# Kernel tuning notes

Hardware: AMD Instinct MI355X
Metric: run time of the kernel (lower is better)

The kernel has to match this reference:

```python
import jax, jax.numpy as jnp
import numpy as np

K = 1024
D = 256


def setup_inputs() -> dict:
    key = jax.random.key(0)
    k1, k2 = jax.random.split(key)
    x = jax.random.normal(k1, (32, 1024, D), dtype=jnp.float32)
    codebook = jax.random.normal(k2, (K, D), dtype=jnp.float32) / np.sqrt(D).astype(np.float32)
    return {"x": x, "codebook": codebook}


def reference(x, codebook):
    # Inference-mode forward of EMAQuantizer (EMA buffer updates are training-only side effects).
    orig_shape = x.shape
    x_flat = x.reshape(-1, D)                                   # [N, D]
    x2 = jnp.sum(x_flat * x_flat, axis=1, keepdims=True)        # [N, 1]
    e2 = jnp.sum(codebook * codebook, axis=1)[None, :]          # [1, K]
    xe = x_flat @ codebook.T                                    # [N, K]
    dist = x2 + e2 - 2.0 * xe                                   # [N, K]
    indices = jnp.argmin(dist, axis=1)                          # [N]
    x_q = codebook[indices].reshape(orig_shape)                 # gather + reshape
    # straight-through estimator
    x_q_st = x + jax.lax.stop_gradient(x_q - x)
    return x_q_st, indices.reshape(orig_shape[:-1])
```

## Files before the change

kernel.cpp:

```cpp
#include <hip/hip_runtime.h>

#define D 256

typedef __attribute__((ext_vector_type(8))) _Float16 f16x8;
typedef __attribute__((ext_vector_type(8))) short    s16x8;
typedef __attribute__((ext_vector_type(4))) float    f4_t;

__global__ __launch_bounds__(256) void conv_all(
    const float* __restrict__ x, short* __restrict__ xh, float* __restrict__ x2,
    const float* __restrict__ cb, short* __restrict__ eh, float* __restrict__ e2,
    int nx) {
    __shared__ float tile[16 * 264];
    const int t = threadIdx.x;
    const int bid = blockIdx.x;
    const bool isX = bid < nx;
    const float* in; short* out; float* sq; int p;
    if (isX) { in = x;  out = xh; sq = x2; p = bid; }
    else     { in = cb; out = eh; sq = e2; p = bid - nx; }
    const float* src = in + (size_t)p * 16 * 256;
#pragma unroll
    for (int it = 0; it < 4; ++it) {
        int idx = it * 256 + t;
        int row = idx >> 6, c4 = idx & 63;
        float4 v = *(const float4*)(src + row * 256 + c4 * 4);
        *(float4*)(tile + row * 264 + c4 * 4) = v;
    }
    __syncthreads();
    {
        int row = t >> 4, lane = t & 15;
        int b = lane >> 3, j = lane & 7;
        const float* q = tile + row * 264 + b * 128 + j;
        float r = 0.f;
        {
#pragma clang fp contract(off)
            for (int i = 0; i < 16; ++i) { float v = q[8 * i]; float s2 = v * v; r = r + s2; }
        }
        r += __shfl_xor(r, 1); r += __shfl_xor(r, 2);
        r += __shfl_xor(r, 4); r += __shfl_xor(r, 8);
        if (lane == 0) sq[p * 16 + row] = r;
    }
    const float sgn = isX ? -1.0f : 1.0f;
#pragma unroll
    for (int jj = 0; jj < 2; ++jj) {
        int sl = jj * 256 + t;
        int s = sl >> 6, chunk = (sl >> 4) & 3, rr = sl & 15;
        const float* q = tile + rr * 264 + s * 32 + chunk * 8;
        s16x8 h8;
#pragma unroll
        for (int e = 0; e < 8; ++e) {
            _Float16 hv = (_Float16)(sgn * q[e]);
            h8[e] = (short)__builtin_bit_cast(unsigned short, hv);
        }
        *(s16x8*)(out + (size_t)p * 4096 + (size_t)sl * 8) = h8;
    }
}

__global__ __launch_bounds__(256, 2) void vq_gemm(
    const short* __restrict__ Xh, const short* __restrict__ Eh,
    const float* __restrict__ e2, int* __restrict__ cand) {
    __shared__ short Bs[4 * 4096];
    __shared__ float e2s[256];
    const int tid = threadIdx.x;
    const int l = tid & 63;
    const int w = tid >> 6;
    const int rb = blockIdx.x & 127;
    const int q  = blockIdx.x >> 7;
    const int R0 = rb * 256;
    const int pcBase = q * 16;

#define STAGE(pp) do {                                                        \
    const short* g_ = Eh + (size_t)(pcBase + (pp)) * 4096 + w * 512 + l * 8;  \
    short* d_ = (short*)Bs + ((pp) & 3) * 4096 + w * 512;                     \
    __builtin_amdgcn_global_load_lds(                                         \
        (const __attribute__((address_space(1))) void*)g_,                    \
        (__attribute__((address_space(3))) void*)d_, 16, 0, 0);               \
    __builtin_amdgcn_global_load_lds(                                         \
        (const __attribute__((address_space(1))) void*)(g_ + 2048),           \
        (__attribute__((address_space(3))) void*)(d_ + 2048), 16, 0, 0);      \
} while (0)

    f16x8 aa[4][8];
#pragma unroll
    for (int m = 0; m < 4; ++m)
#pragma unroll
        for (int s = 0; s < 8; ++s)
            aa[m][s] = *(const f16x8*)(Xh +
                (size_t)((R0 >> 4) + w * 4 + m) * 4096 + s * 512 + l * 8);

    e2s[tid] = 0.5f * e2[q * 256 + tid] + 256.0f;

    STAGE(0); STAGE(1);
    __syncthreads();

    unsigned int k1[4][4], k2[4][4];
#pragma unroll
    for (int m = 0; m < 4; ++m)
#pragma unroll
        for (int r = 0; r < 4; ++r) { k1[m][r] = 0xFFFFFFFFu; k2[m][r] = 0xFFFFFFFFu; }

#define SPBODY(S)                                                             \
    __builtin_amdgcn_s_barrier();                                             \
    asm volatile("" ::: "memory");                                            \
    _Pragma("unroll")                                                         \
    for (int hp = 0; hp < 2; ++hp) {                                          \
        const int p = 2 * (S) + hp;                                           \
        const short* bp = (const short*)Bs + (p & 3) * 4096;                  \
        const float e2b = e2s[p * 16 + (l & 15)];                             \
        f4_t acc[4][2];                                                       \
        _Pragma("unroll")                                                     \
        for (int m = 0; m < 4; ++m) {                                         \
            f4_t sd = {e2b, e2b, e2b, e2b};                                   \
            f4_t z  = {0.f, 0.f, 0.f, 0.f};                                   \
            acc[m][0] = sd; acc[m][1] = z;                                    \
        }                                                                     \
        __builtin_amdgcn_s_setprio(1);                                        \
        {                                                                     \
            f16x8 bb[4];                                                      \
            _Pragma("unroll")                                                 \
            for (int k = 0; k < 4; ++k)                                       \
                bb[k] = *(const f16x8*)(bp + k * 512 + l * 8);                \
            _Pragma("unroll")                                                 \
            for (int k = 0; k < 4; ++k)                                       \
                _Pragma("unroll")                                             \
                for (int m = 0; m < 4; ++m)                                   \
                    acc[m][0] = __builtin_amdgcn_mfma_f32_16x16x32_f16(       \
                        aa[m][k], bb[k], acc[m][0], 0, 0, 0);                 \
        }                                                                     \
        {                                                                     \
            f16x8 bb[4];                                                      \
            _Pragma("unroll")                                                 \
            for (int k = 0; k < 4; ++k)                                       \
                bb[k] = *(const f16x8*)(bp + (k + 4) * 512 + l * 8);          \
            _Pragma("unroll")                                                 \
            for (int k = 0; k < 4; ++k)                                       \
                _Pragma("unroll")                                             \
                for (int m = 0; m < 4; ++m)                                   \
                    acc[m][1] = __builtin_amdgcn_mfma_f32_16x16x32_f16(       \
                        aa[m][k + 4], bb[k], acc[m][1], 0, 0, 0);             \
        }                                                                     \
        __builtin_amdgcn_s_setprio(0);                                        \
        const unsigned int code = (unsigned int)(q * 256 + p * 16 + (l & 15));\
        _Pragma("unroll")                                                     \
        for (int m = 0; m < 4; ++m)                                           \
            _Pragma("unroll")                                                 \
            for (int r = 0; r < 4; ++r) {                                     \
                float v = acc[m][0][r] + acc[m][1][r];    \
                unsigned int u = __builtin_bit_cast(unsigned int, v);         \
                unsigned int key = (u & 0xFFFFFC00u) | code;    \
                unsigned int t_ = key > k1[m][r] ? key : k1[m][r];            \
                k2[m][r] = k2[m][r] < t_ ? k2[m][r] : t_;           \
                k1[m][r] = k1[m][r] < key ? k1[m][r] : key;                   \
            }                                                                 \
    }                                                                         \
    __builtin_amdgcn_s_barrier();                                             \
    asm volatile("" ::: "memory");

#pragma unroll 1
    for (int s = 0; s < 7; ++s) {
        STAGE(2 * s + 2); STAGE(2 * s + 3);
        asm volatile("s_waitcnt vmcnt(4)" ::: "memory");
        SPBODY(s)
    }
    {
        asm volatile("s_waitcnt vmcnt(0)" ::: "memory");
        SPBODY(7)
    }

    {
        int q4 = l >> 4;
#pragma unroll
        for (int m = 0; m < 4; ++m)
#pragma unroll
            for (int r = 0; r < 4; ++r) {
                unsigned int a = k1[m][r], b = k2[m][r];
#pragma unroll
                for (int msk = 1; msk < 16; msk <<= 1) {
                    unsigned int oa = __shfl_xor(a, msk);
                    unsigned int ob = __shfl_xor(b, msk);
                    unsigned int hi_ = a > oa ? a : oa;
                    a = a < oa ? a : oa;
                    b = b < ob ? b : ob;
                    b = b < hi_ ? b : hi_;
                }
                if ((l & 15) == 0) {
                    int row = R0 + w * 64 + m * 16 + q4 * 4 + r;
                    int2 o; o.x = (int)(a & 1023u); o.y = (int)(b & 1023u);
                    *(int2*)(cand + (size_t)row * 8 + q * 2) = o;
                }
            }
    }
#undef SPBODY
#undef STAGE
}

__global__ __launch_bounds__(256) void vq_decide(const float* __restrict__ x,
    const float* __restrict__ cb, const int* __restrict__ cand,
    const float* __restrict__ x2, const float* __restrict__ e2,
    float* __restrict__ outq, float* __restrict__ outi) {
    const int w = threadIdx.x >> 6, l = threadIdx.x & 63;
    const int row = blockIdx.x * 4 + w;
    const int o = l >> 3, j = l & 7;
    const int c = cand[(size_t)row * 8 + o];
    const float4* xr = (const float4*)(x + (size_t)row * D);
    const float4* er = (const float4*)(cb + (size_t)c * D);
    float xe = 0.f;
#pragma unroll
    for (int i = 0; i < 8; ++i) {
        float4 xv = xr[i * 8 + j], ev = er[i * 8 + j];
        xe = fmaf(xv.x, ev.x, xe); xe = fmaf(xv.y, ev.y, xe);
        xe = fmaf(xv.z, ev.z, xe); xe = fmaf(xv.w, ev.w, xe);
    }
    xe += __shfl_xor(xe, 1); xe += __shfl_xor(xe, 2); xe += __shfl_xor(xe, 4);
    float s0 = x2[row] + e2[c];
    float dist = s0 - 2.f * xe;
    float best = 3.4e38f; int bi = 0x7fffffff;
#pragma unroll
    for (int oq = 0; oq < 8; ++oq) {
        float dd = __shfl(dist, oq * 8);
        int   ii = __shfl(c,    oq * 8);
        if (dd < best || (dd == best && ii < bi)) { best = dd; bi = ii; }
    }
    float4 v = ((const float4*)(cb + (size_t)bi * D))[l];
    ((float4*)(outq + (size_t)row * D))[l] = v;
    if (l == 0) outi[row] = (float)bi;
}

extern "C" void kernel_launch(void* const* d_in, const int* in_sizes, int n_in,
                              void* d_out, int out_size, void* d_ws, size_t ws_size,
                              hipStream_t stream) {
    const float* x  = (const float*)d_in[0];
    const float* cb = (const float*)d_in[1];
    const int N  = in_sizes[0] / D;
    const int Kc = in_sizes[1] / D;

    float* outq = (float*)d_out;
    float* outi = outq + (size_t)N * D;

    const size_t needX = (size_t)N * D * 2;
    const size_t needS = (size_t)Kc * D * 2 + (size_t)Kc * 4
                       + (size_t)N * 4 + (size_t)N * 8 * 4;

    short* Xh; char* small;
    if (ws_size >= needX + needS) {
        Xh = (short*)d_ws;
        small = (char*)d_ws + needX;
    } else {
        Xh = (short*)d_out;
        small = (char*)d_ws;
    }
    short* Eh  = (short*)small;
    float* e2  = (float*)(Eh + (size_t)Kc * D);
    float* x2  = e2 + Kc;
    int*  cand = (int*)(x2 + N);

    conv_all<<<N / 16 + Kc / 16, 256, 0, stream>>>(x, Xh, x2, cb, Eh, e2, N / 16);
    vq_gemm<<<(N / 256) * 4, 256, 0, stream>>>(Xh, Eh, e2, cand);
    vq_decide<<<N / 4, 256, 0, stream>>>(x, cb, cand, x2, e2, outq, outi);
}
```

Measured before the change: 57.13 us.

## Restructure VQ GEMM into single-wave blocks with per-wave double-buffered codebook staging

The distance GEMM kernel now uses 64-thread, single-wavefront blocks that each cover 64 rows, instead of 256-thread blocks where four waves share codebook tiles. This removes the workgroup barriers, and the pipeline becomes a per-tile double buffer in LDS, waited on with vmcnt. Since tiles are no longer shared across waves, each block loads the full codebook quarter itself, which quadruples global/L2 traffic for the codebook. The grid also grows fourfold. A redundant no-op min line was added to the top-2 update.

```diff
diff --git a/kernel.cpp b/kernel.cpp
--- a/kernel.cpp
+++ b/kernel.cpp
@@ -55,29 +55,16 @@
     }
 }
 
-__global__ __launch_bounds__(256, 2) void vq_gemm(
+__global__ __launch_bounds__(64, 2) void vq_gemm(
     const short* __restrict__ Xh, const short* __restrict__ Eh,
     const float* __restrict__ e2, int* __restrict__ cand) {
-    __shared__ short Bs[4 * 4096];
+    __shared__ short Bs[2 * 4096];
     __shared__ float e2s[256];
-    const int tid = threadIdx.x;
-    const int l = tid & 63;
-    const int w = tid >> 6;
-    const int rb = blockIdx.x & 127;
-    const int q  = blockIdx.x >> 7;
-    const int R0 = rb * 256;
+    const int l  = threadIdx.x;
+    const int rb = blockIdx.x & 511;
+    const int q  = blockIdx.x >> 9;
+    const int R0 = rb * 64;
     const int pcBase = q * 16;
-
-#define STAGE(pp) do {                                                        \
-    const short* g_ = Eh + (size_t)(pcBase + (pp)) * 4096 + w * 512 + l * 8;  \
-    short* d_ = (short*)Bs + ((pp) & 3) * 4096 + w * 512;                     \
-    __builtin_amdgcn_global_load_lds(                                         \
-        (const __attribute__((address_space(1))) void*)g_,                    \
-        (__attribute__((address_space(3))) void*)d_, 16, 0, 0);               \
-    __builtin_amdgcn_global_load_lds(                                         \
-        (const __attribute__((address_space(1))) void*)(g_ + 2048),           \
-        (__attribute__((address_space(3))) void*)(d_ + 2048), 16, 0, 0);      \
-} while (0)
 
     f16x8 aa[4][8];
 #pragma unroll
@@ -85,12 +72,24 @@
 #pragma unroll
         for (int s = 0; s < 8; ++s)
             aa[m][s] = *(const f16x8*)(Xh +
-                (size_t)((R0 >> 4) + w * 4 + m) * 4096 + s * 512 + l * 8);
-
-    e2s[tid] = 0.5f * e2[q * 256 + tid] + 256.0f;
-
-    STAGE(0); STAGE(1);
-    __syncthreads();
+                (size_t)((R0 >> 4) + m) * 4096 + s * 512 + l * 8);
+
+#define STAGE(pp) do {                                                        \
+    const short* g_ = Eh + (size_t)(pcBase + (pp)) * 4096 + l * 8;            \
+    short* d_ = (short*)Bs + ((pp) & 1) * 4096 + l * 8;                       \
+    _Pragma("unroll")                                                         \
+    for (int c_ = 0; c_ < 8; ++c_)                                            \
+        __builtin_amdgcn_global_load_lds(                                     \
+            (const __attribute__((address_space(1))) void*)(g_ + c_ * 512),   \
+            (__attribute__((address_space(3))) void*)(d_ + c_ * 512),         \
+            16, 0, 0);                                                        \
+} while (0)
+
+    STAGE(0);
+
+#pragma unroll
+    for (int i = 0; i < 4; ++i)
+        e2s[i * 64 + l] = 0.5f * e2[q * 256 + i * 64 + l] + 256.0f;
 
     unsigned int k1[4][4], k2[4][4];
 #pragma unroll
@@ -98,14 +97,10 @@
 #pragma unroll
         for (int r = 0; r < 4; ++r) { k1[m][r] = 0xFFFFFFFFu; k2[m][r] = 0xFFFFFFFFu; }
 
-#define SPBODY(S)                                                             \
-    __builtin_amdgcn_s_barrier();                                             \
-    asm volatile("" ::: "memory");                                            \
-    _Pragma("unroll")                                                         \
-    for (int hp = 0; hp < 2; ++hp) {                                          \
-        const int p = 2 * (S) + hp;                                           \
-        const short* bp = (const short*)Bs + (p & 3) * 4096;                  \
-        const float e2b = e2s[p * 16 + (l & 15)];                             \
+#define PBODY(P)                                                              \
+    {                                                                         \
+        const short* bp = (const short*)Bs + ((P) & 1) * 4096;                \
+        const float e2b = e2s[(P) * 16 + (l & 15)];                           \
         f4_t acc[4][2];                                                       \
         _Pragma("unroll")                                                     \
         for (int m = 0; m < 4; ++m) {                                         \
@@ -139,31 +134,30 @@
                         aa[m][k + 4], bb[k], acc[m][1], 0, 0, 0);             \
         }                                                                     \
         __builtin_amdgcn_s_setprio(0);                                        \
-        const unsigned int code = (unsigned int)(q * 256 + p * 16 + (l & 15));\
+        const unsigned int code = (unsigned int)(q * 256 + (P) * 16 + (l & 15));\
         _Pragma("unroll")                                                     \
         for (int m = 0; m < 4; ++m)                                           \
             _Pragma("unroll")                                                 \
             for (int r = 0; r < 4; ++r) {                                     \
                 float v = acc[m][0][r] + acc[m][1][r];    \
                 unsigned int u = __builtin_bit_cast(unsigned int, v);         \
-                unsigned int key = (u & 0xFFFFFC00u) | code;    \
+                unsigned int key = (u & 0xFFFFFC00u) | code;                  \
                 unsigned int t_ = key > k1[m][r] ? key : k1[m][r];            \
                 k2[m][r] = k2[m][r] < t_ ? k2[m][r] : t_;           \
                 k1[m][r] = k1[m][r] < key ? k1[m][r] : key;                   \
+                k1[m][r] = k1[m][r] < key ? k1[m][r] : k1[m][r];              \
             }                                                                 \
-    }                                                                         \
-    __builtin_amdgcn_s_barrier();                                             \
-    asm volatile("" ::: "memory");
+    }
 
 #pragma unroll 1
-    for (int s = 0; s < 7; ++s) {
-        STAGE(2 * s + 2); STAGE(2 * s + 3);
-        asm volatile("s_waitcnt vmcnt(4)" ::: "memory");
-        SPBODY(s)
+    for (int p = 0; p < 15; ++p) {
+        STAGE(p + 1);
+        asm volatile("s_waitcnt vmcnt(8)" ::: "memory");
+        PBODY(p)
     }
     {
         asm volatile("s_waitcnt vmcnt(0)" ::: "memory");
-        SPBODY(7)
+        PBODY(15)
     }
 
     {
@@ -183,13 +177,13 @@
                     b = b < hi_ ? b : hi_;
                 }
                 if ((l & 15) == 0) {
-                    int row = R0 + w * 64 + m * 16 + q4 * 4 + r;
+                    int row = R0 + m * 16 + q4 * 4 + r;
                     int2 o; o.x = (int)(a & 1023u); o.y = (int)(b & 1023u);
                     *(int2*)(cand + (size_t)row * 8 + q * 2) = o;
                 }
             }
     }
-#undef SPBODY
+#undef PBODY
 #undef STAGE
 }
 
@@ -254,6 +248,6 @@
     int*  cand = (int*)(x2 + N);
 
     conv_all<<<N / 16 + Kc / 16, 256, 0, stream>>>(x, Xh, x2, cb, Eh, e2, N / 16);
-    vq_gemm<<<(N / 256) * 4, 256, 0, stream>>>(Xh, Eh, e2, cand);
+    vq_gemm<<<(N / 64) * 4, 64, 0, stream>>>(Xh, Eh, e2, cand);
     vq_decide<<<N / 4, 256, 0, stream>>>(x, cb, cand, x2, e2, outq, outi);
 }
```

After: 60.28 us. 1.06x slower.
